# Performance work log

Measured on AMD Instinct MI355X. Metric: run time of the kernel, lower is better.

The kernel has to match this reference:

```python
import jax, jax.numpy as jnp
import numpy as np

N = 50000      # nodes in current tree level
N_CH = 3       # actual children present in mailbox
D = 4          # max_output_degree
H = 256        # h_size


def setup_inputs() -> dict:
    key = jax.random.key(0)
    ks = jax.random.split(key, 6)
    return {
        "neighbour_h": jax.random.normal(ks[0], (N, N_CH, H), dtype=jnp.float32),
        "neighbour_c": jax.random.normal(ks[1], (N, N_CH, H), dtype=jnp.float32),
        "f_input": jax.random.normal(ks[2], (N, H), dtype=jnp.float32),
        "iou_input": jax.random.normal(ks[3], (N, 3 * H), dtype=jnp.float32),
        # torch nn.Linear convention: weight [out, in]; one per child position
        "U_f": jax.random.normal(ks[4], (D, H, H), dtype=jnp.float32) * 0.05,
        "U_iou": jax.random.normal(ks[5], (D, 3 * H, H), dtype=jnp.float32) * 0.05,
    }


def reference(neighbour_h, neighbour_c, f_input, iou_input, U_f, U_iou):
    n, n_ch, h = neighbour_h.shape
    d = U_f.shape[0]
    pad = d - n_ch
    # check_missing_children: pad with bottom_h / bottom_c == zeros
    nh = jnp.pad(neighbour_h, ((0, 0), (0, pad), (0, 0)))  # [N, D, H]
    nc = jnp.pad(neighbour_c, ((0, 0), (0, pad), (0, 0)))  # [N, D, H]
    # per-position forget gates: U_f_i @ h_i, plus f_input repeated per child
    f_logits = jnp.einsum('ndh,dkh->ndk', nh, U_f) + f_input[:, None, :]
    # iou gate (canonical n-ary tree-LSTM): sum_i U_iou_i @ h_i, plus iou_input
    iou_aggr = jnp.einsum('ndh,dkh->nk', nh, U_iou) + iou_input  # [N, 3H]
    f = jax.nn.sigmoid(f_logits)
    c_aggr = jnp.sum(f * nc, axis=1)  # [N, H]
    # apply_node_func: iou = iou_input + iou_aggr (iou_input counted twice, as in source)
    iou = iou_input + iou_aggr
    i, o, u = jnp.split(iou, 3, axis=1)
    c = jax.nn.sigmoid(i) * jnp.tanh(u) + c_aggr
    h_out = jax.nn.sigmoid(o) * jnp.tanh(c)
    return (h_out, c)
```

## Files before the change

kernel.cpp:

```cpp
#include <hip/hip_runtime.h>
#include <cstdint>
#include <cstddef>

#define NNODES 50000
#define HD 256
#define NCH 3

typedef __attribute__((ext_vector_type(8))) short shortx8;
typedef __attribute__((ext_vector_type(4))) float floatx4;

__device__ __forceinline__ unsigned short f2bf(float x) {
    union { float f; uint32_t u; } v; v.f = x;
    uint32_t r = v.u + 0x7fffu + ((v.u >> 16) & 1u);
    return (unsigned short)(r >> 16);
}

__device__ __forceinline__ float sigf(float x) {
    return 1.0f / (1.0f + __expf(-x));
}
__device__ __forceinline__ float tanhfast(float x) {
    return 1.0f - 2.0f / (__expf(2.0f * x) + 1.0f);
}

__device__ __forceinline__ floatx4 mfma16(shortx8 a, shortx8 b, floatx4 c) {
    return __builtin_amdgcn_mfma_f32_16x16x32_bf16(a, b, c, 0, 0, 0);
}

__global__ void prep_weights(const float* __restrict__ U_f,
                             const float* __restrict__ U_iou,
                             unsigned short* __restrict__ wsB) {
    int idx = blockIdx.x * 256 + threadIdx.x;
    int lane = idx & 63;
    int ks   = (idx >> 6) & 7;
    int tile = (idx >> 9) & 63;
    int d    = idx >> 15;
    if (d >= NCH) return;
    int col = tile * 16 + (lane & 15);
    int k0  = ks * 32 + (lane >> 4) * 8;
    const float* src = (col < 256)
        ? (U_f   + (((size_t)d * 256 + col)         * 256 + k0))
        : (U_iou + (((size_t)d * 768 + (col - 256)) * 256 + k0));
    shortx8 o;
    #pragma unroll
    for (int e = 0; e < 8; ++e) o[e] = (short)f2bf(src[e]);
    reinterpret_cast<shortx8*>(wsB)[idx] = o;
}

__global__ __launch_bounds__(1024) void treelstm_main(
    const float* __restrict__ nh,
    const float* __restrict__ ncc,
    const float* __restrict__ f_in,
    const float* __restrict__ iou_in,
    const unsigned short* __restrict__ wsB,
    float* __restrict__ out)
{
    extern __shared__ char smem[];
    unsigned short* sA = (unsigned short*)smem;
    float*          sF = (float*)(smem + 32768);

    const int tid  = threadIdx.x;
    const int nb   = blockIdx.x * 64;
    const int lane = tid & 63;
    const int w    = tid >> 6;
    const int cl   = lane & 15;
    const int g    = lane >> 4;

    const shortx8* Bfr = reinterpret_cast<const shortx8*>(wsB);

    float4 fin_r[4];
    float4 cagg[4];
    floatx4 accIOU[4][3];
    #pragma unroll
    for (int i = 0; i < 4; ++i) cagg[i] = float4{0.f, 0.f, 0.f, 0.f};
    #pragma unroll
    for (int rt = 0; rt < 4; ++rt)
        #pragma unroll
        for (int s = 0; s < 3; ++s)
            #pragma unroll
            for (int e = 0; e < 4; ++e) accIOU[rt][s][e] = 0.0f;

    for (int d = 0; d < NCH; ++d) {
        __syncthreads();
        #pragma unroll
        for (int i = 0; i < 2; ++i) {
            int c    = i * 1024 + tid;
            int node = c >> 5;
            int slot = c & 31;
            int gn   = nb + node;
            shortx8 o;
            if (gn < NNODES) {
                const float4* q = reinterpret_cast<const float4*>(
                    nh + ((size_t)gn * (NCH * HD) + d * HD + slot * 8));
                float4 u0 = q[0], u1 = q[1];
                o[0] = (short)f2bf(u0.x); o[1] = (short)f2bf(u0.y);
                o[2] = (short)f2bf(u0.z); o[3] = (short)f2bf(u0.w);
                o[4] = (short)f2bf(u1.x); o[5] = (short)f2bf(u1.y);
                o[6] = (short)f2bf(u1.z); o[7] = (short)f2bf(u1.w);
            } else {
                #pragma unroll
                for (int e = 0; e < 8; ++e) o[e] = 0;
            }
            *reinterpret_cast<shortx8*>(&sA[(slot * 64 + node) * 8]) = o;
        }
        __syncthreads();

        floatx4 accF[4];
        #pragma unroll
        for (int rt = 0; rt < 4; ++rt)
            #pragma unroll
            for (int e = 0; e < 4; ++e) accF[rt][e] = 0.0f;

        #pragma unroll 2
        for (int ks = 0; ks < 8; ++ks) {
            int an = (ks * 4 + g) * 64 + cl;
            shortx8 a0 = *reinterpret_cast<const shortx8*>(&sA[an * 8]);
            shortx8 a1 = *reinterpret_cast<const shortx8*>(&sA[(an + 16) * 8]);
            shortx8 a2 = *reinterpret_cast<const shortx8*>(&sA[(an + 32) * 8]);
            shortx8 a3 = *reinterpret_cast<const shortx8*>(&sA[(an + 48) * 8]);
            shortx8 bF = Bfr[((d * 64 +      w) * 8 + ks) * 64 + lane];
            shortx8 bI = Bfr[((d * 64 + 16 + w) * 8 + ks) * 64 + lane];
            shortx8 bO = Bfr[((d * 64 + 32 + w) * 8 + ks) * 64 + lane];
            shortx8 bU = Bfr[((d * 64 + 48 + w) * 8 + ks) * 64 + lane];
            accF[0] = mfma16(a0, bF, accF[0]);
            accF[1] = mfma16(a1, bF, accF[1]);
            accF[2] = mfma16(a2, bF, accF[2]);
            accF[3] = mfma16(a3, bF, accF[3]);
            accIOU[0][0] = mfma16(a0, bI, accIOU[0][0]);
            accIOU[1][0] = mfma16(a1, bI, accIOU[1][0]);
            accIOU[2][0] = mfma16(a2, bI, accIOU[2][0]);
            accIOU[3][0] = mfma16(a3, bI, accIOU[3][0]);
            accIOU[0][1] = mfma16(a0, bO, accIOU[0][1]);
            accIOU[1][1] = mfma16(a1, bO, accIOU[1][1]);
            accIOU[2][1] = mfma16(a2, bO, accIOU[2][1]);
            accIOU[3][1] = mfma16(a3, bO, accIOU[3][1]);
            accIOU[0][2] = mfma16(a0, bU, accIOU[0][2]);
            accIOU[1][2] = mfma16(a1, bU, accIOU[1][2]);
            accIOU[2][2] = mfma16(a2, bU, accIOU[2][2]);
            accIOU[3][2] = mfma16(a3, bU, accIOU[3][2]);
        }

        #pragma unroll
        for (int rt = 0; rt < 4; ++rt)
            #pragma unroll
            for (int r = 0; r < 4; ++r)
                sF[(rt * 16 + g * 4 + r) * 256 + w * 16 + cl] = accF[rt][r];
        __syncthreads();

        #pragma unroll
        for (int i = 0; i < 4; ++i) {
            int e    = (i * 1024 + tid) * 4;
            int node = e >> 8;
            int k    = e & 255;
            int gn   = nb + node;
            if (gn < NNODES) {
                float4 Fv = *reinterpret_cast<float4*>(&sF[node * 256 + k]);
                if (d == 0)
                    fin_r[i] = *reinterpret_cast<const float4*>(
                        f_in + (size_t)gn * HD + k);
                float4 nc = *reinterpret_cast<const float4*>(
                    ncc + (size_t)gn * (NCH * HD) + d * HD + k);
                cagg[i].x += sigf(Fv.x + fin_r[i].x) * nc.x;
                cagg[i].y += sigf(Fv.y + fin_r[i].y) * nc.y;
                cagg[i].z += sigf(Fv.z + fin_r[i].z) * nc.z;
                cagg[i].w += sigf(Fv.w + fin_r[i].w) * nc.w;
            }
        }
    }

    float4 ii[4], cc2[4];

    __syncthreads();
    #pragma unroll
    for (int rt = 0; rt < 4; ++rt)
        #pragma unroll
        for (int r = 0; r < 4; ++r)
            sF[(rt * 16 + g * 4 + r) * 256 + w * 16 + cl] = accIOU[rt][0][r];
    __syncthreads();
    #pragma unroll
    for (int i = 0; i < 4; ++i) {
        int e = (i * 1024 + tid) * 4, node = e >> 8, k = e & 255;
        int gn = nb + node;
        if (gn < NNODES) {
            float4 v  = *reinterpret_cast<float4*>(&sF[node * 256 + k]);
            float4 io = *reinterpret_cast<const float4*>(
                iou_in + (size_t)gn * 768 + k);
            ii[i].x = v.x + 2.0f * io.x; ii[i].y = v.y + 2.0f * io.y;
            ii[i].z = v.z + 2.0f * io.z; ii[i].w = v.w + 2.0f * io.w;
        }
    }

    __syncthreads();
    #pragma unroll
    for (int rt = 0; rt < 4; ++rt)
        #pragma unroll
        for (int r = 0; r < 4; ++r)
            sF[(rt * 16 + g * 4 + r) * 256 + w * 16 + cl] = accIOU[rt][2][r];
    __syncthreads();
    #pragma unroll
    for (int i = 0; i < 4; ++i) {
        int e = (i * 1024 + tid) * 4, node = e >> 8, k = e & 255;
        int gn = nb + node;
        if (gn < NNODES) {
            float4 v  = *reinterpret_cast<float4*>(&sF[node * 256 + k]);
            float4 io = *reinterpret_cast<const float4*>(
                iou_in + (size_t)gn * 768 + 512 + k);
            cc2[i].x = sigf(ii[i].x) * tanhfast(v.x + 2.0f * io.x) + cagg[i].x;
            cc2[i].y = sigf(ii[i].y) * tanhfast(v.y + 2.0f * io.y) + cagg[i].y;
            cc2[i].z = sigf(ii[i].z) * tanhfast(v.z + 2.0f * io.z) + cagg[i].z;
            cc2[i].w = sigf(ii[i].w) * tanhfast(v.w + 2.0f * io.w) + cagg[i].w;
        }
    }

    __syncthreads();
    #pragma unroll
    for (int rt = 0; rt < 4; ++rt)
        #pragma unroll
        for (int r = 0; r < 4; ++r)
            sF[(rt * 16 + g * 4 + r) * 256 + w * 16 + cl] = accIOU[rt][1][r];
    __syncthreads();
    #pragma unroll
    for (int i = 0; i < 4; ++i) {
        int e = (i * 1024 + tid) * 4, node = e >> 8, k = e & 255;
        int gn = nb + node;
        if (gn < NNODES) {
            float4 v  = *reinterpret_cast<float4*>(&sF[node * 256 + k]);
            float4 io = *reinterpret_cast<const float4*>(
                iou_in + (size_t)gn * 768 + 256 + k);
            float4 hh;
            hh.x = sigf(v.x + 2.0f * io.x) * tanhfast(cc2[i].x);
            hh.y = sigf(v.y + 2.0f * io.y) * tanhfast(cc2[i].y);
            hh.z = sigf(v.z + 2.0f * io.z) * tanhfast(cc2[i].z);
            hh.w = sigf(v.w + 2.0f * io.w) * tanhfast(cc2[i].w);
            *reinterpret_cast<float4*>(out + (size_t)gn * HD + k) = hh;
            *reinterpret_cast<float4*>(out + (size_t)(NNODES + gn) * HD + k) = cc2[i];
        }
    }
}

extern "C" void kernel_launch(void* const* d_in, const int* in_sizes, int n_in,
                              void* d_out, int out_size, void* d_ws, size_t ws_size,
                              hipStream_t stream) {
    const float* nh     = (const float*)d_in[0];
    const float* ncc    = (const float*)d_in[1];
    const float* f_in   = (const float*)d_in[2];
    const float* iou_in = (const float*)d_in[3];
    const float* U_f    = (const float*)d_in[4];
    const float* U_iou  = (const float*)d_in[5];
    unsigned short* wsB = (unsigned short*)d_ws;

    if (ws_size < (size_t)(3 * 64 * 8 * 64) * 16) return;

    hipLaunchKernelGGL(prep_weights, dim3(384), dim3(256), 0, stream,
                       U_f, U_iou, wsB);
    hipLaunchKernelGGL(treelstm_main, dim3((NNODES + 63) / 64), dim3(1024),
                       98304, stream, nh, ncc, f_in, iou_in, wsB, (float*)d_out);
}
```

Before: 323.5 us.

## Shrink block to 32 nodes, stage all children upfront, use bf16 LDS staging

Blocks now cover 32 nodes with 512 threads instead of 64 nodes with 1024, so several blocks can share a CU. All three children's h are converted and staged in LDS once at the start. The forget-gate GEMM is split from the IOU GEMM, which runs in a second pass. Accumulators are written to LDS as bf16 instead of fp32, and neighbour_c and iou_input loads are issued before the barriers. This aims to cut LDS use, register pressure and sync stalls so loads overlap compute, at the cost of extra bf16 rounding of the gate pre-activations and more weight fetches per node.

```diff
diff --git a/kernel.cpp b/kernel.cpp
--- a/kernel.cpp
+++ b/kernel.cpp
@@ -5,6 +5,7 @@
 #define NNODES 50000
 #define HD 256
 #define NCH 3
+#define BM 32
 
 typedef __attribute__((ext_vector_type(8))) short shortx8;
 typedef __attribute__((ext_vector_type(4))) float floatx4;
@@ -14,14 +15,15 @@
     uint32_t r = v.u + 0x7fffu + ((v.u >> 16) & 1u);
     return (unsigned short)(r >> 16);
 }
-
+__device__ __forceinline__ float bf2f(unsigned short u) {
+    union { uint32_t u; float f; } v; v.u = ((uint32_t)u) << 16; return v.f;
+}
 __device__ __forceinline__ float sigf(float x) {
     return 1.0f / (1.0f + __expf(-x));
 }
 __device__ __forceinline__ float tanhfast(float x) {
     return 1.0f - 2.0f / (__expf(2.0f * x) + 1.0f);
 }
-
 __device__ __forceinline__ floatx4 mfma16(shortx8 a, shortx8 b, floatx4 c) {
     return __builtin_amdgcn_mfma_f32_16x16x32_bf16(a, b, c, 0, 0, 0);
 }
@@ -46,7 +48,7 @@
     reinterpret_cast<shortx8*>(wsB)[idx] = o;
 }
 
-__global__ __launch_bounds__(1024) void treelstm_main(
+__global__ __launch_bounds__(512, 4) void treelstm_main(
     const float* __restrict__ nh,
     const float* __restrict__ ncc,
     const float* __restrict__ f_in,
@@ -54,12 +56,11 @@
     const unsigned short* __restrict__ wsB,
     float* __restrict__ out)
 {
-    extern __shared__ char smem[];
-    unsigned short* sA = (unsigned short*)smem;
-    float*          sF = (float*)(smem + 32768);
+    __shared__ unsigned short sA[NCH * 32 * BM * 8];
+    __shared__ unsigned short sF[BM * 256];
 
     const int tid  = threadIdx.x;
-    const int nb   = blockIdx.x * 64;
+    const int nb   = blockIdx.x * BM;
     const int lane = tid & 63;
     const int w    = tid >> 6;
     const int cl   = lane & 15;
@@ -67,170 +68,212 @@
 
     const shortx8* Bfr = reinterpret_cast<const shortx8*>(wsB);
 
+    #pragma unroll
+    for (int i = 0; i < 6; ++i) {
+        int c    = i * 512 + tid;
+        int d    = c >> 10;
+        int node = (c >> 5) & 31;
+        int slot = c & 31;
+        int gn   = nb + node;
+        shortx8 o;
+        if (gn < NNODES) {
+            const float4* q = reinterpret_cast<const float4*>(
+                nh + ((size_t)gn * (NCH * HD) + d * HD + slot * 8));
+            float4 u0 = q[0], u1 = q[1];
+            o[0] = (short)f2bf(u0.x); o[1] = (short)f2bf(u0.y);
+            o[2] = (short)f2bf(u0.z); o[3] = (short)f2bf(u0.w);
+            o[4] = (short)f2bf(u1.x); o[5] = (short)f2bf(u1.y);
+            o[6] = (short)f2bf(u1.z); o[7] = (short)f2bf(u1.w);
+        } else {
+            #pragma unroll
+            for (int e = 0; e < 8; ++e) o[e] = 0;
+        }
+        *reinterpret_cast<shortx8*>(&sA[((d * 32 + slot) * BM + node) * 8]) = o;
+    }
+    __syncthreads();
+
     float4 fin_r[4];
     float4 cagg[4];
-    floatx4 accIOU[4][3];
     #pragma unroll
     for (int i = 0; i < 4; ++i) cagg[i] = float4{0.f, 0.f, 0.f, 0.f};
-    #pragma unroll
-    for (int rt = 0; rt < 4; ++rt)
-        #pragma unroll
-        for (int s = 0; s < 3; ++s)
-            #pragma unroll
-            for (int e = 0; e < 4; ++e) accIOU[rt][s][e] = 0.0f;
 
     for (int d = 0; d < NCH; ++d) {
-        __syncthreads();
-        #pragma unroll
-        for (int i = 0; i < 2; ++i) {
-            int c    = i * 1024 + tid;
-            int node = c >> 5;
-            int slot = c & 31;
-            int gn   = nb + node;
-            shortx8 o;
+        float4 ncr[4];
+        #pragma unroll
+        for (int i = 0; i < 4; ++i) {
+            int e = (i * 512 + tid) * 4, node = e >> 8, k = e & 255;
+            int gn = nb + node;
             if (gn < NNODES) {
-                const float4* q = reinterpret_cast<const float4*>(
-                    nh + ((size_t)gn * (NCH * HD) + d * HD + slot * 8));
-                float4 u0 = q[0], u1 = q[1];
-                o[0] = (short)f2bf(u0.x); o[1] = (short)f2bf(u0.y);
-                o[2] = (short)f2bf(u0.z); o[3] = (short)f2bf(u0.w);
-                o[4] = (short)f2bf(u1.x); o[5] = (short)f2bf(u1.y);
-                o[6] = (short)f2bf(u1.z); o[7] = (short)f2bf(u1.w);
-            } else {
-                #pragma unroll
-                for (int e = 0; e < 8; ++e) o[e] = 0;
-            }
-            *reinterpret_cast<shortx8*>(&sA[(slot * 64 + node) * 8]) = o;
-        }
-        __syncthreads();
-
-        floatx4 accF[4];
-        #pragma unroll
-        for (int rt = 0; rt < 4; ++rt)
-            #pragma unroll
-            for (int e = 0; e < 4; ++e) accF[rt][e] = 0.0f;
-
-        #pragma unroll 2
-        for (int ks = 0; ks < 8; ++ks) {
-            int an = (ks * 4 + g) * 64 + cl;
-            shortx8 a0 = *reinterpret_cast<const shortx8*>(&sA[an * 8]);
-            shortx8 a1 = *reinterpret_cast<const shortx8*>(&sA[(an + 16) * 8]);
-            shortx8 a2 = *reinterpret_cast<const shortx8*>(&sA[(an + 32) * 8]);
-            shortx8 a3 = *reinterpret_cast<const shortx8*>(&sA[(an + 48) * 8]);
-            shortx8 bF = Bfr[((d * 64 +      w) * 8 + ks) * 64 + lane];
-            shortx8 bI = Bfr[((d * 64 + 16 + w) * 8 + ks) * 64 + lane];
-            shortx8 bO = Bfr[((d * 64 + 32 + w) * 8 + ks) * 64 + lane];
-            shortx8 bU = Bfr[((d * 64 + 48 + w) * 8 + ks) * 64 + lane];
-            accF[0] = mfma16(a0, bF, accF[0]);
-            accF[1] = mfma16(a1, bF, accF[1]);
-            accF[2] = mfma16(a2, bF, accF[2]);
-            accF[3] = mfma16(a3, bF, accF[3]);
-            accIOU[0][0] = mfma16(a0, bI, accIOU[0][0]);
-            accIOU[1][0] = mfma16(a1, bI, accIOU[1][0]);
-            accIOU[2][0] = mfma16(a2, bI, accIOU[2][0]);
-            accIOU[3][0] = mfma16(a3, bI, accIOU[3][0]);
-            accIOU[0][1] = mfma16(a0, bO, accIOU[0][1]);
-            accIOU[1][1] = mfma16(a1, bO, accIOU[1][1]);
-            accIOU[2][1] = mfma16(a2, bO, accIOU[2][1]);
-            accIOU[3][1] = mfma16(a3, bO, accIOU[3][1]);
-            accIOU[0][2] = mfma16(a0, bU, accIOU[0][2]);
-            accIOU[1][2] = mfma16(a1, bU, accIOU[1][2]);
-            accIOU[2][2] = mfma16(a2, bU, accIOU[2][2]);
-            accIOU[3][2] = mfma16(a3, bU, accIOU[3][2]);
-        }
-
-        #pragma unroll
-        for (int rt = 0; rt < 4; ++rt)
-            #pragma unroll
-            for (int r = 0; r < 4; ++r)
-                sF[(rt * 16 + g * 4 + r) * 256 + w * 16 + cl] = accF[rt][r];
-        __syncthreads();
-
-        #pragma unroll
-        for (int i = 0; i < 4; ++i) {
-            int e    = (i * 1024 + tid) * 4;
-            int node = e >> 8;
-            int k    = e & 255;
-            int gn   = nb + node;
-            if (gn < NNODES) {
-                float4 Fv = *reinterpret_cast<float4*>(&sF[node * 256 + k]);
+                ncr[i] = *reinterpret_cast<const float4*>(
+                    ncc + (size_t)gn * (NCH * HD) + d * HD + k);
                 if (d == 0)
                     fin_r[i] = *reinterpret_cast<const float4*>(
                         f_in + (size_t)gn * HD + k);
-                float4 nc = *reinterpret_cast<const float4*>(
-                    ncc + (size_t)gn * (NCH * HD) + d * HD + k);
-                cagg[i].x += sigf(Fv.x + fin_r[i].x) * nc.x;
-                cagg[i].y += sigf(Fv.y + fin_r[i].y) * nc.y;
-                cagg[i].z += sigf(Fv.z + fin_r[i].z) * nc.z;
-                cagg[i].w += sigf(Fv.w + fin_r[i].w) * nc.w;
             }
         }
-    }
-
-    float4 ii[4], cc2[4];
-
-    __syncthreads();
-    #pragma unroll
-    for (int rt = 0; rt < 4; ++rt)
-        #pragma unroll
-        for (int r = 0; r < 4; ++r)
-            sF[(rt * 16 + g * 4 + r) * 256 + w * 16 + cl] = accIOU[rt][0][r];
-    __syncthreads();
-    #pragma unroll
-    for (int i = 0; i < 4; ++i) {
-        int e = (i * 1024 + tid) * 4, node = e >> 8, k = e & 255;
+
+        floatx4 accF[2][2];
+        #pragma unroll
+        for (int rt = 0; rt < 2; ++rt)
+            #pragma unroll
+            for (int j = 0; j < 2; ++j)
+                #pragma unroll
+                for (int e = 0; e < 4; ++e) accF[rt][j][e] = 0.0f;
+
+        #pragma unroll
+        for (int ks = 0; ks < 8; ++ks) {
+            int an = (d * 32 + ks * 4 + g) * BM + cl;
+            shortx8 a0 = *reinterpret_cast<const shortx8*>(&sA[an * 8]);
+            shortx8 a1 = *reinterpret_cast<const shortx8*>(&sA[(an + 16) * 8]);
+            shortx8 b0 = Bfr[((d * 64 + 2 * w)     * 8 + ks) * 64 + lane];
+            shortx8 b1 = Bfr[((d * 64 + 2 * w + 1) * 8 + ks) * 64 + lane];
+            accF[0][0] = mfma16(a0, b0, accF[0][0]);
+            accF[1][0] = mfma16(a1, b0, accF[1][0]);
+            accF[0][1] = mfma16(a0, b1, accF[0][1]);
+            accF[1][1] = mfma16(a1, b1, accF[1][1]);
+        }
+
+        __syncthreads();
+        #pragma unroll
+        for (int rt = 0; rt < 2; ++rt)
+            #pragma unroll
+            for (int j = 0; j < 2; ++j)
+                #pragma unroll
+                for (int r = 0; r < 4; ++r)
+                    sF[(rt * 16 + g * 4 + r) * 256 + w * 32 + j * 16 + cl] =
+                        f2bf(accF[rt][j][r]);
+        __syncthreads();
+
+        #pragma unroll
+        for (int i = 0; i < 4; ++i) {
+            int e = (i * 512 + tid) * 4, node = e >> 8, k = e & 255;
+            int gn = nb + node;
+            if (gn < NNODES) {
+                ushort4 Fb = *reinterpret_cast<ushort4*>(&sF[node * 256 + k]);
+                cagg[i].x += sigf(bf2f(Fb.x) + fin_r[i].x) * ncr[i].x;
+                cagg[i].y += sigf(bf2f(Fb.y) + fin_r[i].y) * ncr[i].y;
+                cagg[i].z += sigf(bf2f(Fb.z) + fin_r[i].z) * ncr[i].z;
+                cagg[i].w += sigf(bf2f(Fb.w) + fin_r[i].w) * ncr[i].w;
+            }
+        }
+    }
+
+    floatx4 acc[2][6];
+    #pragma unroll
+    for (int rt = 0; rt < 2; ++rt)
+        #pragma unroll
+        for (int q = 0; q < 6; ++q)
+            #pragma unroll
+            for (int e = 0; e < 4; ++e) acc[rt][q][e] = 0.0f;
+
+    for (int d = 0; d < NCH; ++d) {
+        #pragma unroll
+        for (int ks = 0; ks < 8; ++ks) {
+            int an = (d * 32 + ks * 4 + g) * BM + cl;
+            shortx8 a0 = *reinterpret_cast<const shortx8*>(&sA[an * 8]);
+            shortx8 a1 = *reinterpret_cast<const shortx8*>(&sA[(an + 16) * 8]);
+            #pragma unroll
+            for (int q = 0; q < 3; ++q) {
+                shortx8 b0 = Bfr[((d * 64 + 16 + q * 16 + 2 * w)     * 8 + ks) * 64 + lane];
+                shortx8 b1 = Bfr[((d * 64 + 16 + q * 16 + 2 * w + 1) * 8 + ks) * 64 + lane];
+                acc[0][q * 2 + 0] = mfma16(a0, b0, acc[0][q * 2 + 0]);
+                acc[1][q * 2 + 0] = mfma16(a1, b0, acc[1][q * 2 + 0]);
+                acc[0][q * 2 + 1] = mfma16(a0, b1, acc[0][q * 2 + 1]);
+                acc[1][q * 2 + 1] = mfma16(a1, b1, acc[1][q * 2 + 1]);
+            }
+        }
+    }
+
+    float4 ii[4], cc2[4], iol[4];
+
+    #pragma unroll
+    for (int i = 0; i < 4; ++i) {
+        int e = (i * 512 + tid) * 4, node = e >> 8, k = e & 255;
+        int gn = nb + node;
+        if (gn < NNODES)
+            iol[i] = *reinterpret_cast<const float4*>(iou_in + (size_t)gn * 768 + k);
+    }
+    __syncthreads();
+    #pragma unroll
+    for (int rt = 0; rt < 2; ++rt)
+        #pragma unroll
+        for (int j = 0; j < 2; ++j)
+            #pragma unroll
+            for (int r = 0; r < 4; ++r)
+                sF[(rt * 16 + g * 4 + r) * 256 + w * 32 + j * 16 + cl] =
+                    f2bf(acc[rt][j][r]);
+    __syncthreads();
+    #pragma unroll
+    for (int i = 0; i < 4; ++i) {
+        int e = (i * 512 + tid) * 4, node = e >> 8, k = e & 255;
         int gn = nb + node;
         if (gn < NNODES) {
-            float4 v  = *reinterpret_cast<float4*>(&sF[node * 256 + k]);
-            float4 io = *reinterpret_cast<const float4*>(
-                iou_in + (size_t)gn * 768 + k);
-            ii[i].x = v.x + 2.0f * io.x; ii[i].y = v.y + 2.0f * io.y;
-            ii[i].z = v.z + 2.0f * io.z; ii[i].w = v.w + 2.0f * io.w;
-        }
-    }
-
-    __syncthreads();
-    #pragma unroll
-    for (int rt = 0; rt < 4; ++rt)
-        #pragma unroll
-        for (int r = 0; r < 4; ++r)
-            sF[(rt * 16 + g * 4 + r) * 256 + w * 16 + cl] = accIOU[rt][2][r];
-    __syncthreads();
-    #pragma unroll
-    for (int i = 0; i < 4; ++i) {
-        int e = (i * 1024 + tid) * 4, node = e >> 8, k = e & 255;
+            ushort4 Vb = *reinterpret_cast<ushort4*>(&sF[node * 256 + k]);
+            ii[i].x = bf2f(Vb.x) + 2.0f * iol[i].x;
+            ii[i].y = bf2f(Vb.y) + 2.0f * iol[i].y;
+            ii[i].z = bf2f(Vb.z) + 2.0f * iol[i].z;
+            ii[i].w = bf2f(Vb.w) + 2.0f * iol[i].w;
+        }
+    }
+
+    #pragma unroll
+    for (int i = 0; i < 4; ++i) {
+        int e = (i * 512 + tid) * 4, node = e >> 8, k = e & 255;
+        int gn = nb + node;
+        if (gn < NNODES)
+            iol[i] = *reinterpret_cast<const float4*>(iou_in + (size_t)gn * 768 + 512 + k);
+    }
+    __syncthreads();
+    #pragma unroll
+    for (int rt = 0; rt < 2; ++rt)
+        #pragma unroll
+        for (int j = 0; j < 2; ++j)
+            #pragma unroll
+            for (int r = 0; r < 4; ++r)
+                sF[(rt * 16 + g * 4 + r) * 256 + w * 32 + j * 16 + cl] =
+                    f2bf(acc[rt][4 + j][r]);
+    __syncthreads();
+    #pragma unroll
+    for (int i = 0; i < 4; ++i) {
+        int e = (i * 512 + tid) * 4, node = e >> 8, k = e & 255;
         int gn = nb + node;
         if (gn < NNODES) {
-            float4 v  = *reinterpret_cast<float4*>(&sF[node * 256 + k]);
-            float4 io = *reinterpret_cast<const float4*>(
-                iou_in + (size_t)gn * 768 + 512 + k);
-            cc2[i].x = sigf(ii[i].x) * tanhfast(v.x + 2.0f * io.x) + cagg[i].x;
-            cc2[i].y = sigf(ii[i].y) * tanhfast(v.y + 2.0f * io.y) + cagg[i].y;
-            cc2[i].z = sigf(ii[i].z) * tanhfast(v.z + 2.0f * io.z) + cagg[i].z;
-            cc2[i].w = sigf(ii[i].w) * tanhfast(v.w + 2.0f * io.w) + cagg[i].w;
-        }
-    }
-
-    __syncthreads();
-    #pragma unroll
-    for (int rt = 0; rt < 4; ++rt)
-        #pragma unroll
-        for (int r = 0; r < 4; ++r)
-            sF[(rt * 16 + g * 4 + r) * 256 + w * 16 + cl] = accIOU[rt][1][r];
-    __syncthreads();
-    #pragma unroll
-    for (int i = 0; i < 4; ++i) {
-        int e = (i * 1024 + tid) * 4, node = e >> 8, k = e & 255;
+            ushort4 Vb = *reinterpret_cast<ushort4*>(&sF[node * 256 + k]);
+            cc2[i].x = sigf(ii[i].x) * tanhfast(bf2f(Vb.x) + 2.0f * iol[i].x) + cagg[i].x;
+            cc2[i].y = sigf(ii[i].y) * tanhfast(bf2f(Vb.y) + 2.0f * iol[i].y) + cagg[i].y;
+            cc2[i].z = sigf(ii[i].z) * tanhfast(bf2f(Vb.z) + 2.0f * iol[i].z) + cagg[i].z;
+            cc2[i].w = sigf(ii[i].w) * tanhfast(bf2f(Vb.w) + 2.0f * iol[i].w) + cagg[i].w;
+        }
+    }
+
+    #pragma unroll
+    for (int i = 0; i < 4; ++i) {
+        int e = (i * 512 + tid) * 4, node = e >> 8, k = e & 255;
+        int gn = nb + node;
+        if (gn < NNODES)
+            iol[i] = *reinterpret_cast<const float4*>(iou_in + (size_t)gn * 768 + 256 + k);
+    }
+    __syncthreads();
+    #pragma unroll
+    for (int rt = 0; rt < 2; ++rt)
+        #pragma unroll
+        for (int j = 0; j < 2; ++j)
+            #pragma unroll
+            for (int r = 0; r < 4; ++r)
+                sF[(rt * 16 + g * 4 + r) * 256 + w * 32 + j * 16 + cl] =
+                    f2bf(acc[rt][2 + j][r]);
+    __syncthreads();
+    #pragma unroll
+    for (int i = 0; i < 4; ++i) {
+        int e = (i * 512 + tid) * 4, node = e >> 8, k = e & 255;
         int gn = nb + node;
         if (gn < NNODES) {
-            float4 v  = *reinterpret_cast<float4*>(&sF[node * 256 + k]);
-            float4 io = *reinterpret_cast<const float4*>(
-                iou_in + (size_t)gn * 768 + 256 + k);
+            ushort4 Vb = *reinterpret_cast<ushort4*>(&sF[node * 256 + k]);
             float4 hh;
-            hh.x = sigf(v.x + 2.0f * io.x) * tanhfast(cc2[i].x);
-            hh.y = sigf(v.y + 2.0f * io.y) * tanhfast(cc2[i].y);
-            hh.z = sigf(v.z + 2.0f * io.z) * tanhfast(cc2[i].z);
-            hh.w = sigf(v.w + 2.0f * io.w) * tanhfast(cc2[i].w);
+            hh.x = sigf(bf2f(Vb.x) + 2.0f * iol[i].x) * tanhfast(cc2[i].x);
+            hh.y = sigf(bf2f(Vb.y) + 2.0f * iol[i].y) * tanhfast(cc2[i].y);
+            hh.z = sigf(bf2f(Vb.z) + 2.0f * iol[i].z) * tanhfast(cc2[i].z);
+            hh.w = sigf(bf2f(Vb.w) + 2.0f * iol[i].w) * tanhfast(cc2[i].w);
             *reinterpret_cast<float4*>(out + (size_t)gn * HD + k) = hh;
             *reinterpret_cast<float4*>(out + (size_t)(NNODES + gn) * HD + k) = cc2[i];
         }
@@ -252,6 +295,6 @@
 
     hipLaunchKernelGGL(prep_weights, dim3(384), dim3(256), 0, stream,
                        U_f, U_iou, wsB);
-    hipLaunchKernelGGL(treelstm_main, dim3((NNODES + 63) / 64), dim3(1024),
-                       98304, stream, nh, ncc, f_in, iou_in, wsB, (float*)d_out);
-}
+    hipLaunchKernelGGL(treelstm_main, dim3((NNODES + BM - 1) / BM), dim3(512),
+                       0, stream, nh, ncc, f_in, iou_in, wsB, (float*)d_out);
+}
```

After: 307.2 us. 1.05x faster.
